# Optimization experiments

Measured on AMD Instinct MI355X. Metric: run time of the kernel, lower is better.

## Reference

```python
import jax, jax.numpy as jnp
import numpy as np

C = 1.0          # Poincare ball curvature
H = 8            # num_heads
EPS = 1e-15
DELTA = 1e-7
SC = np.sqrt(C)  # sqrt curvature


def _norm(x):
    return jnp.sqrt(jnp.clip(jnp.sum(x * x, -1, keepdims=True), 1e-15))


def mobius_add(x, y):
    xy = jnp.sum(x * y, -1, keepdims=True)
    x2 = jnp.sum(x * x, -1, keepdims=True)
    y2 = jnp.sum(y * y, -1, keepdims=True)
    num = (1 + 2 * C * xy + C * y2) * x + (1 - C * x2) * y
    den = 1 + 2 * C * xy + C * C * x2 * y2
    return num / (den + EPS)


def mobius_matvec(W, x):
    xn = _norm(x)
    mx = x @ W.T
    mxn = _norm(mx)
    arg = jnp.clip(SC * xn, None, 1 - 1e-5)
    return jnp.tanh(mxn / xn * jnp.arctanh(arg)) * mx / (mxn * SC)


def logmap0(x):
    xn = _norm(x)
    return jnp.arctanh(jnp.clip(SC * xn, None, 1 - 1e-5)) * x / (SC * xn)


def expmap0(u):
    un = _norm(u)
    return jnp.tanh(SC * un) * u / (SC * un)


def hyp_linear(W, b, x):
    return mobius_add(mobius_matvec(W, x), b)


def setup_inputs() -> dict:
    key = jax.random.key(0)
    ks = jax.random.split(key, 5)
    B, S, E = 2, 512, 256
    x = jax.random.normal(ks[0], (B, S, E), jnp.float32) * 0.02  # inside unit ball
    scale = float(np.sqrt(6.0 / (E + E)))  # xavier uniform bound
    Wq = jax.random.uniform(ks[1], (E, E), jnp.float32, -scale, scale)
    Wk = jax.random.uniform(ks[2], (E, E), jnp.float32, -scale, scale)
    Wv = jax.random.uniform(ks[3], (E, E), jnp.float32, -scale, scale)
    Wo = jax.random.uniform(ks[4], (E, E), jnp.float32, -scale, scale)
    z = jnp.zeros((E,), jnp.float32)
    head_scaling = jnp.ones((H, 1, 1), jnp.float32)
    return {"x": x, "Wq": Wq, "bq": z, "Wk": Wk, "bk": z, "Wv": Wv, "bv": z,
            "Wo": Wo, "bo": z, "head_scaling": head_scaling}


def reference(x, Wq, bq, Wk, bk, Wv, bv, Wo, bo, head_scaling):
    B, S, E = x.shape
    D = E // H
    q = hyp_linear(Wq, bq, x).reshape(B, S, H, D).transpose(0, 2, 1, 3)  # (B,H,S,D)
    k = hyp_linear(Wk, bk, x).reshape(B, S, H, D).transpose(0, 2, 1, 3)
    v = hyp_linear(Wv, bv, x).reshape(B, S, H, D).transpose(0, 2, 1, 3)
    max_norm = (1 - 1e-5) / SC
    q = jnp.minimum(q, max_norm)  # elementwise clamp_max, faithful to source
    k = jnp.minimum(k, max_norm)
    qn = C * jnp.sum(q * q, -1)[..., :, None]   # (B,H,Sq,1)
    kn = C * jnp.sum(k * k, -1)[..., None, :]   # (B,H,1,Sk)
    # pairwise mobius_add(-k, q): (B,H,Sq,Sk,D)
    diff = mobius_add(-k[:, :, None, :, :], q[:, :, :, None, :])
    dn = C * jnp.sum(diff * diff, -1)           # (B,H,Sq,Sk)
    denom = (1 - qn) * (1 - kn) + EPS
    a = jnp.maximum(1 + 2 * dn / denom, 1 + DELTA)
    dist = jnp.log(a + jnp.sqrt(a * a - 1))     # acosh
    scores = -dist / (head_scaling * np.sqrt(D))
    w = jax.nn.softmax(scores, -1)
    out = expmap0(jnp.einsum('bhqk,bhkd->bhqd', w, logmap0(v)))
    out = out.transpose(0, 2, 1, 3).reshape(B, S, E)
    return hyp_linear(Wo, bo, out)
```

## Files before the change

kernel.cpp:

```cpp
#include <hip/hip_runtime.h>
#include <math.h>

#define Ec 256
#define Sc 512
#define Bc 2
#define Hc 8
#define Dc 32
#define MAXNORM (1.0f - 1e-5f)
#define NEc (Bc * Sc * Ec)
#define KSPLIT 2
#define NROWS (Bc * Hc * Sc)

__device__ __forceinline__ float fullWaveSum(float v) {
#pragma unroll
  for (int m = 32; m >= 1; m >>= 1) v += __shfl_xor(v, m, 64);
  return v;
}
__device__ __forceinline__ float halfWaveSum(float v) {
#pragma unroll
  for (int m = 16; m >= 1; m >>= 1) v += __shfl_xor(v, m, 64);
  return v;
}
__device__ __forceinline__ float atanh_fast(float z) {
  return 0.5f * __logf((1.0f + z) / (1.0f - z));
}
__device__ __forceinline__ float tanh_fast(float a) {
  float e = __expf(-2.0f * a);
  return (1.0f - e) / (1.0f + e);
}

__global__ __launch_bounds__(128) void gemm_xwt(
    const float* __restrict__ X,
    const float* __restrict__ W0, const float* __restrict__ W1,
    const float* __restrict__ W2,
    float* __restrict__ O0, float* __restrict__ O1, float* __restrict__ O2) {
  const int tid = threadIdx.x;
  const int bx = blockIdx.x;
  const int by = blockIdx.y;
  const int kz = blockIdx.z;
  const int mat = by >> 2;
  const int cb0 = (by & 3) * 64;
  const int rb0 = bx * 32;
  const float* __restrict__ W = (mat == 0) ? W0 : (mat == 1) ? W1 : W2;
  float* __restrict__ O = ((mat == 0) ? O0 : (mat == 1) ? O1 : O2) + (size_t)kz * NEc;

  __shared__ float Xs[64][36];
  __shared__ float Ws[64][68];

  const int f4 = tid & 15;
  const int sub = tid >> 4;
  const int ty = tid >> 4;
  const int tx = tid & 15;

  float acc[4][4];
#pragma unroll
  for (int i = 0; i < 4; ++i)
#pragma unroll
    for (int j = 0; j < 4; ++j) acc[i][j] = 0.f;

  for (int kk = kz * 128; kk < kz * 128 + 128; kk += 64) {
    __syncthreads();
#pragma unroll
    for (int i = 0; i < 4; ++i) {
      int row = sub + i * 8;
      float4 v = *(const float4*)&X[(size_t)(rb0 + row) * Ec + kk + f4 * 4];
      Xs[f4 * 4 + 0][row] = v.x;
      Xs[f4 * 4 + 1][row] = v.y;
      Xs[f4 * 4 + 2][row] = v.z;
      Xs[f4 * 4 + 3][row] = v.w;
    }
#pragma unroll
    for (int i = 0; i < 8; ++i) {
      int col = sub + i * 8;
      float4 v = *(const float4*)&W[(size_t)(cb0 + col) * Ec + kk + f4 * 4];
      Ws[f4 * 4 + 0][col] = v.x;
      Ws[f4 * 4 + 1][col] = v.y;
      Ws[f4 * 4 + 2][col] = v.z;
      Ws[f4 * 4 + 3][col] = v.w;
    }
    __syncthreads();
#pragma unroll 8
    for (int k = 0; k < 64; ++k) {
      float4 a = *(const float4*)&Xs[k][ty * 4];
      float4 b = *(const float4*)&Ws[k][tx * 4];
      float av[4] = {a.x, a.y, a.z, a.w};
      float bv[4] = {b.x, b.y, b.z, b.w};
#pragma unroll
      for (int i = 0; i < 4; ++i)
#pragma unroll
        for (int j = 0; j < 4; ++j) acc[i][j] = fmaf(av[i], bv[j], acc[i][j]);
    }
  }
#pragma unroll
  for (int i = 0; i < 4; ++i) {
    float4 o = make_float4(acc[i][0], acc[i][1], acc[i][2], acc[i][3]);
    *(float4*)&O[(size_t)(rb0 + ty * 4 + i) * Ec + cb0 + tx * 4] = o;
  }
}

__global__ __launch_bounds__(256) void qkv_stats(
    const float* __restrict__ x,
    const float* __restrict__ mxq, const float* __restrict__ mxk,
    const float* __restrict__ mxv,
    const float* __restrict__ bq, const float* __restrict__ bk,
    const float* __restrict__ bv,
    float* __restrict__ qo, float* __restrict__ ko, float* __restrict__ lvo,
    float* __restrict__ qno, float* __restrict__ kno) {
  const int t = threadIdx.x;
  const int row = blockIdx.x;
  const int b = row >> 9;
  const int s = row & (Sc - 1);
  const size_t idx = (size_t)row * Ec + t;
  const float xv = x[idx];
  float mq = 0.f, mk = 0.f, mv = 0.f;
#pragma unroll
  for (int p = 0; p < KSPLIT; ++p) {
    mq += mxq[idx + (size_t)p * NEc];
    mk += mxk[idx + (size_t)p * NEc];
    mv += mxv[idx + (size_t)p * NEc];
  }
  const float bb[3] = {bq[t], bk[t], bv[t]};
  const float mvals[3] = {mq, mk, mv};

  float vals[10] = {xv * xv,
                    mq * mq, mq * bb[0], bb[0] * bb[0],
                    mk * mk, mk * bb[1], bb[1] * bb[1],
                    mv * mv, mv * bb[2], bb[2] * bb[2]};
  __shared__ float red[10][4];
  __shared__ float fin[10];
#pragma unroll
  for (int i = 0; i < 10; ++i) {
    float v = fullWaveSum(vals[i]);
    if ((t & 63) == 0) red[i][t >> 6] = v;
  }
  __syncthreads();
  if (t < 10) fin[t] = red[t][0] + red[t][1] + red[t][2] + red[t][3];
  __syncthreads();

  const float x2 = fin[0];
  const float xn = sqrtf(fmaxf(x2, 1e-15f));
  const float at = atanh_fast(fminf(xn, MAXNORM));
  const int h = t >> 5;

#pragma unroll
  for (int m = 0; m < 3; ++m) {
    float mx2 = fin[1 + 3 * m];
    float mxb = fin[2 + 3 * m];
    float b2 = fin[3 + 3 * m];
    float mxn = sqrtf(fmaxf(mx2, 1e-15f));
    float scl = tanh_fast((mxn / xn) * at) / mxn;
    float mvv = scl * mvals[m];
    float X2 = scl * scl * mx2;
    float XY = scl * mxb;
    float numc = 1.0f + 2.0f * XY + b2;
    float den = 1.0f + 2.0f * XY + X2 * b2 + 1e-15f;
    float res = (numc * mvv + (1.0f - X2) * bb[m]) / den;
    if (m < 2) {
      res = fminf(res, MAXNORM);
      float s2 = halfWaveSum(res * res);
      if (m == 0) {
        qo[idx] = res;
        if ((t & 31) == 0) qno[(b * Hc + h) * Sc + s] = s2;
      } else {
        ko[idx] = res;
        if ((t & 31) == 0) kno[(b * Hc + h) * Sc + s] = s2;
      }
    } else {
      float vn2 = halfWaveSum(res * res);
      float vn = sqrtf(fmaxf(vn2, 1e-15f));
      float f = atanh_fast(fminf(vn, MAXNORM)) / vn;
      lvo[idx] = f * res;
    }
  }
}

__global__ __launch_bounds__(512) void attn_fused(
    const float* __restrict__ q, const float* __restrict__ k,
    const float* __restrict__ lv, const float* __restrict__ qn,
    const float* __restrict__ kn, const float* __restrict__ hs,
    float* __restrict__ out) {
  const int tid = threadIdx.x;
  const int qt = blockIdx.x;
  const int bh = blockIdx.y;
  const int b = bh >> 3;
  const int h = bh & 7;
  const int sq0 = qt * 32;

  __shared__ float Qs[32][32];
  __shared__ float Ks[256][32];
  __shared__ float lvs[256][36];
  __shared__ float Ps[32][260];
  __shared__ float accm[32][8][32];
  __shared__ float lsb[32][8];

  const int ty = tid >> 6;
  const int tx = tid & 63;
  const int js = tid >> 6;
  const int rg = (tid >> 3) & 7;
  const int dq = tid & 7;

  if (tid < 256) {
    int r = tid >> 3, fd = tid & 7;
    int fsw = fd ^ ((r >> 2) & 7);
    *(float4*)&Qs[r][fsw * 4] =
        *(const float4*)&q[(size_t)(b * Sc + sq0 + r) * Ec + h * Dc + fd * 4];
  }
  const float sinv = -1.0f / (hs[h] * sqrtf((float)Dc));
  float qnv[4];
#pragma unroll
  for (int i = 0; i < 4; ++i) qnv[i] = qn[bh * Sc + sq0 + ty * 4 + i];

  float4 oacc[4];
#pragma unroll
  for (int i = 0; i < 4; ++i) oacc[i] = make_float4(0.f, 0.f, 0.f, 0.f);
  float lsum4[4] = {0.f, 0.f, 0.f, 0.f};

#pragma unroll 1
  for (int kt = 0; kt < 2; ++kt) {
    const int k0 = kt * 256;
    __syncthreads();
#pragma unroll
    for (int i = 0; i < 4; ++i) {
      int qi = tid + i * 512;
      int r = qi >> 3, fd = qi & 7;
      int fsw = fd ^ ((r >> 2) & 7);
      *(float4*)&Ks[r][fsw * 4] =
          *(const float4*)&k[(size_t)(b * Sc + k0 + r) * Ec + h * Dc + fd * 4];
      *(float4*)&lvs[r][fd * 4] =
          *(const float4*)&lv[(size_t)(b * Sc + k0 + r) * Ec + h * Dc + fd * 4];
    }
    float knv[4];
#pragma unroll
    for (int j = 0; j < 4; ++j) knv[j] = kn[bh * Sc + k0 + tx * 4 + j];
    __syncthreads();

    float acc[4][4];
#pragma unroll
    for (int i = 0; i < 4; ++i)
#pragma unroll
      for (int j = 0; j < 4; ++j) acc[i][j] = 0.f;
#pragma unroll
    for (int fd = 0; fd < 8; ++fd) {
      const int qsw = (fd ^ (ty & 7)) * 4;
      const int ksw = (fd ^ (tx & 7)) * 4;
      float4 a[4], bb[4];
#pragma unroll
      for (int i = 0; i < 4; ++i) a[i] = *(const float4*)&Qs[ty * 4 + i][qsw];
#pragma unroll
      for (int j = 0; j < 4; ++j) bb[j] = *(const float4*)&Ks[tx * 4 + j][ksw];
#pragma unroll
      for (int i = 0; i < 4; ++i)
#pragma unroll
        for (int j = 0; j < 4; ++j) {
          acc[i][j] = fmaf(a[i].x, bb[j].x, acc[i][j]);
          acc[i][j] = fmaf(a[i].y, bb[j].y, acc[i][j]);
          acc[i][j] = fmaf(a[i].z, bb[j].z, acc[i][j]);
          acc[i][j] = fmaf(a[i].w, bb[j].w, acc[i][j]);
        }
    }
#pragma unroll
    for (int i = 0; i < 4; ++i) {
      const float q2 = qnv[i];
      const float omq = 1.0f - q2;
      float po[4];
#pragma unroll
      for (int j = 0; j < 4; ++j) {
        const float k2 = knv[j];
        const float kq = acc[i][j];
        const float omk = 1.0f - k2;
        float s2x2 = fmaf(-4.0f, kq, 2.0f * k2 + 2.0f * q2);
        float dden = fmaf(k2, q2, fmaf(-2.0f, kq, 1.0f)) + 1e-15f;
        float Pd = fmaf(dden, omk * omq, 1e-20f);
        float rp = __builtin_amdgcn_rcpf(Pd);
        float tt = fmaxf(s2x2 * rp, 1e-7f);
        float z = (1.0f + tt) + sqrtf(fmaf(tt, tt, tt + tt));
        po[j] = __builtin_amdgcn_exp2f(sinv * __builtin_amdgcn_logf(z));
      }
      float4 o4 = make_float4(po[0], po[1], po[2], po[3]);
      *(float4*)&Ps[ty * 4 + i][tx * 4] = o4;
    }
    __syncthreads();

#pragma unroll
    for (int jq = 0; jq < 8; ++jq) {
      const int j0 = js * 32 + jq * 4;
      float4 p[4], l[4];
#pragma unroll
      for (int i = 0; i < 4; ++i) p[i] = *(const float4*)&Ps[rg * 4 + i][j0];
#pragma unroll
      for (int c = 0; c < 4; ++c) l[c] = *(const float4*)&lvs[j0 + c][dq * 4];
#pragma unroll
      for (int i = 0; i < 4; ++i) {
        lsum4[i] += (p[i].x + p[i].y) + (p[i].z + p[i].w);
        oacc[i].x = fmaf(p[i].x, l[0].x, oacc[i].x);
        oacc[i].y = fmaf(p[i].x, l[0].y, oacc[i].y);
        oacc[i].z = fmaf(p[i].x, l[0].z, oacc[i].z);
        oacc[i].w = fmaf(p[i].x, l[0].w, oacc[i].w);
        oacc[i].x = fmaf(p[i].y, l[1].x, oacc[i].x);
        oacc[i].y = fmaf(p[i].y, l[1].y, oacc[i].y);
        oacc[i].z = fmaf(p[i].y, l[1].z, oacc[i].z);
        oacc[i].w = fmaf(p[i].y, l[1].w, oacc[i].w);
        oacc[i].x = fmaf(p[i].z, l[2].x, oacc[i].x);
        oacc[i].y = fmaf(p[i].z, l[2].y, oacc[i].y);
        oacc[i].z = fmaf(p[i].z, l[2].z, oacc[i].z);
        oacc[i].w = fmaf(p[i].z, l[2].w, oacc[i].w);
        oacc[i].x = fmaf(p[i].w, l[3].x, oacc[i].x);
        oacc[i].y = fmaf(p[i].w, l[3].y, oacc[i].y);
        oacc[i].z = fmaf(p[i].w, l[3].z, oacc[i].z);
        oacc[i].w = fmaf(p[i].w, l[3].w, oacc[i].w);
      }
    }
  }

  __syncthreads();
#pragma unroll
  for (int i = 0; i < 4; ++i)
    *(float4*)&accm[rg * 4 + i][js][dq * 4] = oacc[i];
  if (dq == 0) {
#pragma unroll
    for (int i = 0; i < 4; ++i) lsb[rg * 4 + i][js] = lsum4[i];
  }
  __syncthreads();

  if (tid < 256) {
    const int rw = tid >> 3;
    const int d2 = tid & 7;
    float4 o = make_float4(0.f, 0.f, 0.f, 0.f);
    float ls = 0.f;
#pragma unroll
    for (int g = 0; g < 8; ++g) {
      float4 a4 = *(const float4*)&accm[rw][g][d2 * 4];
      o.x += a4.x; o.y += a4.y; o.z += a4.z; o.w += a4.w;
      ls += lsb[rw][g];
    }
    const float li = 1.0f / ls;
    o.x *= li; o.y *= li; o.z *= li; o.w *= li;
    float un2 = fmaf(o.x, o.x, fmaf(o.y, o.y, fmaf(o.z, o.z, o.w * o.w)));
#pragma unroll
    for (int m = 4; m >= 1; m >>= 1) un2 += __shfl_xor(un2, m, 8);
    float un = sqrtf(fmaxf(un2, 1e-15f));
    float f = tanh_fast(un) / un;
    float4 ov = make_float4(o.x * f, o.y * f, o.z * f, o.w * f);
    *(float4*)&out[(size_t)(b * Sc + sq0 + rw) * Ec + h * Dc + d2 * 4] = ov;
  }
}

__global__ __launch_bounds__(256) void proj_stats(
    const float* __restrict__ xin, const float* __restrict__ mx,
    const float* __restrict__ bo, float* __restrict__ out) {
  const int t = threadIdx.x;
  const int row = blockIdx.x;
  const size_t idx = (size_t)row * Ec + t;
  const float xv = xin[idx];
  float m = 0.f;
#pragma unroll
  for (int p = 0; p < KSPLIT; ++p) m += mx[idx + (size_t)p * NEc];
  const float bb = bo[t];
  float vals[4] = {xv * xv, m * m, m * bb, bb * bb};
  __shared__ float red[4][4];
  __shared__ float fin[4];
#pragma unroll
  for (int i = 0; i < 4; ++i) {
    float v = fullWaveSum(vals[i]);
    if ((t & 63) == 0) red[i][t >> 6] = v;
  }
  __syncthreads();
  if (t < 4) fin[t] = red[t][0] + red[t][1] + red[t][2] + red[t][3];
  __syncthreads();

  float x2 = fin[0], mx2 = fin[1], mxb = fin[2], b2 = fin[3];
  float xn = sqrtf(fmaxf(x2, 1e-15f));
  float mxn = sqrtf(fmaxf(mx2, 1e-15f));
  float scl = tanh_fast((mxn / xn) * atanh_fast(fminf(xn, MAXNORM))) / mxn;
  float mvv = scl * m;
  float X2 = scl * scl * mx2;
  float XY = scl * mxb;
  float numc = 1.0f + 2.0f * XY + b2;
  float den = 1.0f + 2.0f * XY + X2 * b2 + 1e-15f;
  out[idx] = (numc * mvv + (1.0f - X2) * bb) / den;
}

extern "C" void kernel_launch(void* const* d_in, const int* in_sizes, int n_in,
                              void* d_out, int out_size, void* d_ws, size_t ws_size,
                              hipStream_t stream) {
  (void)in_sizes; (void)n_in; (void)out_size; (void)ws_size;
  const float* x  = (const float*)d_in[0];
  const float* Wq = (const float*)d_in[1];
  const float* bq = (const float*)d_in[2];
  const float* Wk = (const float*)d_in[3];
  const float* bk = (const float*)d_in[4];
  const float* Wv = (const float*)d_in[5];
  const float* bv = (const float*)d_in[6];
  const float* Wo = (const float*)d_in[7];
  const float* bo = (const float*)d_in[8];
  const float* hs = (const float*)d_in[9];

  float* ws = (float*)d_ws;
  const int NE = NEc;
  const int NH = NROWS;
  float* mxq = ws;
  float* mxk = mxq + KSPLIT * NE;
  float* mxv = mxk + KSPLIT * NE;
  float* mxo = mxv + KSPLIT * NE;
  float* qb  = mxo + KSPLIT * NE;
  float* kb  = qb + NE;
  float* lvb = kb + NE;
  float* aob = lvb + NE;
  float* qnb = aob + NE;
  float* knb = qnb + NH;

  const int M = Bc * Sc;

  gemm_xwt<<<dim3(M / 32, 12, KSPLIT), 128, 0, stream>>>(x, Wq, Wk, Wv, mxq, mxk, mxv);
  qkv_stats<<<M, 256, 0, stream>>>(x, mxq, mxk, mxv, bq, bk, bv,
                                   qb, kb, lvb, qnb, knb);
  attn_fused<<<dim3(16, 16), 512, 0, stream>>>(qb, kb, lvb, qnb, knb, hs, aob);
  gemm_xwt<<<dim3(M / 32, 4, KSPLIT), 128, 0, stream>>>(aob, Wo, Wo, Wo, mxo, mxo, mxo);
  proj_stats<<<M, 256, 0, stream>>>(aob, mxo, bo, (float*)d_out);
}
```

Before: 125.6 us.

## Fuse all stages into one persistent kernel with software grid barriers

Replaces the five separate kernel launches with a single 256-block persistent kernel that runs the QKV GEMM, QKV stats, attention, output GEMM and output stats as phases separated by atomic-counter grid barriers. The goal is to remove per-launch overhead and the gaps between dependent launches. The split-K layout also changes: the QKV GEMM now does the full K range with no split, the output GEMM uses a 4-way split, and attention works on 128-key tiles so everything fits one shared-memory pool. In exchange, some phases leave threads idle, and correctness depends on all 256 blocks being resident at once, with an extra memset launch to reset the barrier counters.

New measurement: 212.8 us. 69.4% more time.

```diff
diff --git a/kernel.cpp b/kernel.cpp
--- a/kernel.cpp
+++ b/kernel.cpp
@@ -8,8 +8,9 @@
 #define Dc 32
 #define MAXNORM (1.0f - 1e-5f)
 #define NEc (Bc * Sc * Ec)
-#define KSPLIT 2
 #define NROWS (Bc * Hc * Sc)
+#define NBLK 256
+#define KP 4
 
 __device__ __forceinline__ float fullWaveSum(float v) {
 #pragma unroll
@@ -29,96 +30,98 @@
   return (1.0f - e) / (1.0f + e);
 }
 
-__global__ __launch_bounds__(128) void gemm_xwt(
-    const float* __restrict__ X,
-    const float* __restrict__ W0, const float* __restrict__ W1,
-    const float* __restrict__ W2,
-    float* __restrict__ O0, float* __restrict__ O1, float* __restrict__ O2) {
-  const int tid = threadIdx.x;
-  const int bx = blockIdx.x;
-  const int by = blockIdx.y;
-  const int kz = blockIdx.z;
-  const int mat = by >> 2;
-  const int cb0 = (by & 3) * 64;
-  const int rb0 = bx * 32;
-  const float* __restrict__ W = (mat == 0) ? W0 : (mat == 1) ? W1 : W2;
-  float* __restrict__ O = ((mat == 0) ? O0 : (mat == 1) ? O1 : O2) + (size_t)kz * NEc;
-
-  __shared__ float Xs[64][36];
-  __shared__ float Ws[64][68];
-
-  const int f4 = tid & 15;
-  const int sub = tid >> 4;
-  const int ty = tid >> 4;
-  const int tx = tid & 15;
-
+__device__ __forceinline__ void gridBarrier(unsigned* ctr) {
+  __syncthreads();
+  if (threadIdx.x == 0) {
+    __threadfence();
+    __hip_atomic_fetch_add(ctr, 1u, __ATOMIC_RELAXED, __HIP_MEMORY_SCOPE_AGENT);
+    while (__hip_atomic_load(ctr, __ATOMIC_RELAXED, __HIP_MEMORY_SCOPE_AGENT) <
+           (unsigned)NBLK) {
+      __builtin_amdgcn_s_sleep(2);
+    }
+    __threadfence();
+  }
+  __syncthreads();
+}
+
+__device__ __forceinline__ void gemm_tile(
+    const float* __restrict__ X, const float* __restrict__ W,
+    float* __restrict__ O, float* __restrict__ Xs, float* __restrict__ Ws,
+    const int ltid, const int rb0, const int cb0, const int kk0, const int nk,
+    const bool active) {
+  const int f4 = ltid & 15;
+  const int s8 = ltid >> 4;
+  const int ty = ltid >> 4;
+  const int tx = ltid & 15;
   float acc[4][4];
 #pragma unroll
   for (int i = 0; i < 4; ++i)
 #pragma unroll
     for (int j = 0; j < 4; ++j) acc[i][j] = 0.f;
 
-  for (int kk = kz * 128; kk < kz * 128 + 128; kk += 64) {
+  for (int c = 0; c < nk; ++c) {
+    const int kk = kk0 + c * 64;
     __syncthreads();
+    if (active) {
+#pragma unroll
+      for (int i = 0; i < 4; ++i) {
+        int row = s8 + i * 8;
+        float4 v = *(const float4*)&X[(size_t)(rb0 + row) * Ec + kk + f4 * 4];
+        Xs[(f4 * 4 + 0) * 36 + row] = v.x;
+        Xs[(f4 * 4 + 1) * 36 + row] = v.y;
+        Xs[(f4 * 4 + 2) * 36 + row] = v.z;
+        Xs[(f4 * 4 + 3) * 36 + row] = v.w;
+      }
+#pragma unroll
+      for (int i = 0; i < 8; ++i) {
+        int col = s8 + i * 8;
+        float4 v = *(const float4*)&W[(size_t)(cb0 + col) * Ec + kk + f4 * 4];
+        Ws[(f4 * 4 + 0) * 68 + col] = v.x;
+        Ws[(f4 * 4 + 1) * 68 + col] = v.y;
+        Ws[(f4 * 4 + 2) * 68 + col] = v.z;
+        Ws[(f4 * 4 + 3) * 68 + col] = v.w;
+      }
+    }
+    __syncthreads();
+    if (active) {
+#pragma unroll 8
+      for (int k = 0; k < 64; ++k) {
+        float4 a = *(const float4*)&Xs[k * 36 + ty * 4];
+        float4 b = *(const float4*)&Ws[k * 68 + tx * 4];
+        float av[4] = {a.x, a.y, a.z, a.w};
+        float bv[4] = {b.x, b.y, b.z, b.w};
+#pragma unroll
+        for (int i = 0; i < 4; ++i)
+#pragma unroll
+          for (int j = 0; j < 4; ++j) acc[i][j] = fmaf(av[i], bv[j], acc[i][j]);
+      }
+    }
+  }
+  if (active) {
 #pragma unroll
     for (int i = 0; i < 4; ++i) {
-      int row = sub + i * 8;
-      float4 v = *(const float4*)&X[(size_t)(rb0 + row) * Ec + kk + f4 * 4];
-      Xs[f4 * 4 + 0][row] = v.x;
-      Xs[f4 * 4 + 1][row] = v.y;
-      Xs[f4 * 4 + 2][row] = v.z;
-      Xs[f4 * 4 + 3][row] = v.w;
-    }
-#pragma unroll
-    for (int i = 0; i < 8; ++i) {
-      int col = sub + i * 8;
-      float4 v = *(const float4*)&W[(size_t)(cb0 + col) * Ec + kk + f4 * 4];
-      Ws[f4 * 4 + 0][col] = v.x;
-      Ws[f4 * 4 + 1][col] = v.y;
-      Ws[f4 * 4 + 2][col] = v.z;
-      Ws[f4 * 4 + 3][col] = v.w;
-    }
-    __syncthreads();
-#pragma unroll 8
-    for (int k = 0; k < 64; ++k) {
-      float4 a = *(const float4*)&Xs[k][ty * 4];
-      float4 b = *(const float4*)&Ws[k][tx * 4];
-      float av[4] = {a.x, a.y, a.z, a.w};
-      float bv[4] = {b.x, b.y, b.z, b.w};
-#pragma unroll
-      for (int i = 0; i < 4; ++i)
-#pragma unroll
-        for (int j = 0; j < 4; ++j) acc[i][j] = fmaf(av[i], bv[j], acc[i][j]);
-    }
-  }
-#pragma unroll
-  for (int i = 0; i < 4; ++i) {
-    float4 o = make_float4(acc[i][0], acc[i][1], acc[i][2], acc[i][3]);
-    *(float4*)&O[(size_t)(rb0 + ty * 4 + i) * Ec + cb0 + tx * 4] = o;
-  }
-}
-
-__global__ __launch_bounds__(256) void qkv_stats(
+      float4 o = make_float4(acc[i][0], acc[i][1], acc[i][2], acc[i][3]);
+      *(float4*)&O[(size_t)(rb0 + ty * 4 + i) * Ec + cb0 + tx * 4] = o;
+    }
+  }
+}
+
+__device__ __forceinline__ void qkv_stats_row(
     const float* __restrict__ x,
     const float* __restrict__ mxq, const float* __restrict__ mxk,
     const float* __restrict__ mxv,
     const float* __restrict__ bq, const float* __restrict__ bk,
     const float* __restrict__ bv,
     float* __restrict__ qo, float* __restrict__ ko, float* __restrict__ lvo,
-    float* __restrict__ qno, float* __restrict__ kno) {
-  const int t = threadIdx.x;
-  const int row = blockIdx.x;
+    float* __restrict__ qno, float* __restrict__ kno,
+    const int row, const int t, float (*red)[4], float* fin) {
   const int b = row >> 9;
   const int s = row & (Sc - 1);
   const size_t idx = (size_t)row * Ec + t;
   const float xv = x[idx];
-  float mq = 0.f, mk = 0.f, mv = 0.f;
-#pragma unroll
-  for (int p = 0; p < KSPLIT; ++p) {
-    mq += mxq[idx + (size_t)p * NEc];
-    mk += mxk[idx + (size_t)p * NEc];
-    mv += mxv[idx + (size_t)p * NEc];
-  }
+  const float mq = mxq[idx];
+  const float mk = mxk[idx];
+  const float mv = mxv[idx];
   const float bb[3] = {bq[t], bk[t], bv[t]};
   const float mvals[3] = {mq, mk, mv};
 
@@ -126,8 +129,6 @@
                     mq * mq, mq * bb[0], bb[0] * bb[0],
                     mk * mk, mk * bb[1], bb[1] * bb[1],
                     mv * mv, mv * bb[2], bb[2] * bb[2]};
-  __shared__ float red[10][4];
-  __shared__ float fin[10];
 #pragma unroll
   for (int i = 0; i < 10; ++i) {
     float v = fullWaveSum(vals[i]);
@@ -172,193 +173,20 @@
       lvo[idx] = f * res;
     }
   }
-}
-
-__global__ __launch_bounds__(512) void attn_fused(
-    const float* __restrict__ q, const float* __restrict__ k,
-    const float* __restrict__ lv, const float* __restrict__ qn,
-    const float* __restrict__ kn, const float* __restrict__ hs,
-    float* __restrict__ out) {
-  const int tid = threadIdx.x;
-  const int qt = blockIdx.x;
-  const int bh = blockIdx.y;
-  const int b = bh >> 3;
-  const int h = bh & 7;
-  const int sq0 = qt * 32;
-
-  __shared__ float Qs[32][32];
-  __shared__ float Ks[256][32];
-  __shared__ float lvs[256][36];
-  __shared__ float Ps[32][260];
-  __shared__ float accm[32][8][32];
-  __shared__ float lsb[32][8];
-
-  const int ty = tid >> 6;
-  const int tx = tid & 63;
-  const int js = tid >> 6;
-  const int rg = (tid >> 3) & 7;
-  const int dq = tid & 7;
-
-  if (tid < 256) {
-    int r = tid >> 3, fd = tid & 7;
-    int fsw = fd ^ ((r >> 2) & 7);
-    *(float4*)&Qs[r][fsw * 4] =
-        *(const float4*)&q[(size_t)(b * Sc + sq0 + r) * Ec + h * Dc + fd * 4];
-  }
-  const float sinv = -1.0f / (hs[h] * sqrtf((float)Dc));
-  float qnv[4];
-#pragma unroll
-  for (int i = 0; i < 4; ++i) qnv[i] = qn[bh * Sc + sq0 + ty * 4 + i];
-
-  float4 oacc[4];
-#pragma unroll
-  for (int i = 0; i < 4; ++i) oacc[i] = make_float4(0.f, 0.f, 0.f, 0.f);
-  float lsum4[4] = {0.f, 0.f, 0.f, 0.f};
-
-#pragma unroll 1
-  for (int kt = 0; kt < 2; ++kt) {
-    const int k0 = kt * 256;
-    __syncthreads();
-#pragma unroll
-    for (int i = 0; i < 4; ++i) {
-      int qi = tid + i * 512;
-      int r = qi >> 3, fd = qi & 7;
-      int fsw = fd ^ ((r >> 2) & 7);
-      *(float4*)&Ks[r][fsw * 4] =
-          *(const float4*)&k[(size_t)(b * Sc + k0 + r) * Ec + h * Dc + fd * 4];
-      *(float4*)&lvs[r][fd * 4] =
-          *(const float4*)&lv[(size_t)(b * Sc + k0 + r) * Ec + h * Dc + fd * 4];
-    }
-    float knv[4];
-#pragma unroll
-    for (int j = 0; j < 4; ++j) knv[j] = kn[bh * Sc + k0 + tx * 4 + j];
-    __syncthreads();
-
-    float acc[4][4];
-#pragma unroll
-    for (int i = 0; i < 4; ++i)
-#pragma unroll
-      for (int j = 0; j < 4; ++j) acc[i][j] = 0.f;
-#pragma unroll
-    for (int fd = 0; fd < 8; ++fd) {
-      const int qsw = (fd ^ (ty & 7)) * 4;
-      const int ksw = (fd ^ (tx & 7)) * 4;
-      float4 a[4], bb[4];
-#pragma unroll
-      for (int i = 0; i < 4; ++i) a[i] = *(const float4*)&Qs[ty * 4 + i][qsw];
-#pragma unroll
-      for (int j = 0; j < 4; ++j) bb[j] = *(const float4*)&Ks[tx * 4 + j][ksw];
-#pragma unroll
-      for (int i = 0; i < 4; ++i)
-#pragma unroll
-        for (int j = 0; j < 4; ++j) {
-          acc[i][j] = fmaf(a[i].x, bb[j].x, acc[i][j]);
-          acc[i][j] = fmaf(a[i].y, bb[j].y, acc[i][j]);
-          acc[i][j] = fmaf(a[i].z, bb[j].z, acc[i][j]);
-          acc[i][j] = fmaf(a[i].w, bb[j].w, acc[i][j]);
-        }
-    }
-#pragma unroll
-    for (int i = 0; i < 4; ++i) {
-      const float q2 = qnv[i];
-      const float omq = 1.0f - q2;
-      float po[4];
-#pragma unroll
-      for (int j = 0; j < 4; ++j) {
-        const float k2 = knv[j];
-        const float kq = acc[i][j];
-        const float omk = 1.0f - k2;
-        float s2x2 = fmaf(-4.0f, kq, 2.0f * k2 + 2.0f * q2);
-        float dden = fmaf(k2, q2, fmaf(-2.0f, kq, 1.0f)) + 1e-15f;
-        float Pd = fmaf(dden, omk * omq, 1e-20f);
-        float rp = __builtin_amdgcn_rcpf(Pd);
-        float tt = fmaxf(s2x2 * rp, 1e-7f);
-        float z = (1.0f + tt) + sqrtf(fmaf(tt, tt, tt + tt));
-        po[j] = __builtin_amdgcn_exp2f(sinv * __builtin_amdgcn_logf(z));
-      }
-      float4 o4 = make_float4(po[0], po[1], po[2], po[3]);
-      *(float4*)&Ps[ty * 4 + i][tx * 4] = o4;
-    }
-    __syncthreads();
-
-#pragma unroll
-    for (int jq = 0; jq < 8; ++jq) {
-      const int j0 = js * 32 + jq * 4;
-      float4 p[4], l[4];
-#pragma unroll
-      for (int i = 0; i < 4; ++i) p[i] = *(const float4*)&Ps[rg * 4 + i][j0];
-#pragma unroll
-      for (int c = 0; c < 4; ++c) l[c] = *(const float4*)&lvs[j0 + c][dq * 4];
-#pragma unroll
-      for (int i = 0; i < 4; ++i) {
-        lsum4[i] += (p[i].x + p[i].y) + (p[i].z + p[i].w);
-        oacc[i].x = fmaf(p[i].x, l[0].x, oacc[i].x);
-        oacc[i].y = fmaf(p[i].x, l[0].y, oacc[i].y);
-        oacc[i].z = fmaf(p[i].x, l[0].z, oacc[i].z);
-        oacc[i].w = fmaf(p[i].x, l[0].w, oacc[i].w);
-        oacc[i].x = fmaf(p[i].y, l[1].x, oacc[i].x);
-        oacc[i].y = fmaf(p[i].y, l[1].y, oacc[i].y);
-        oacc[i].z = fmaf(p[i].y, l[1].z, oacc[i].z);
-        oacc[i].w = fmaf(p[i].y, l[1].w, oacc[i].w);
-        oacc[i].x = fmaf(p[i].z, l[2].x, oacc[i].x);
-        oacc[i].y = fmaf(p[i].z, l[2].y, oacc[i].y);
-        oacc[i].z = fmaf(p[i].z, l[2].z, oacc[i].z);
-        oacc[i].w = fmaf(p[i].z, l[2].w, oacc[i].w);
-        oacc[i].x = fmaf(p[i].w, l[3].x, oacc[i].x);
-        oacc[i].y = fmaf(p[i].w, l[3].y, oacc[i].y);
-        oacc[i].z = fmaf(p[i].w, l[3].z, oacc[i].z);
-        oacc[i].w = fmaf(p[i].w, l[3].w, oacc[i].w);
-      }
-    }
-  }
-
-  __syncthreads();
-#pragma unroll
-  for (int i = 0; i < 4; ++i)
-    *(float4*)&accm[rg * 4 + i][js][dq * 4] = oacc[i];
-  if (dq == 0) {
-#pragma unroll
-    for (int i = 0; i < 4; ++i) lsb[rg * 4 + i][js] = lsum4[i];
-  }
-  __syncthreads();
-
-  if (tid < 256) {
-    const int rw = tid >> 3;
-    const int d2 = tid & 7;
-    float4 o = make_float4(0.f, 0.f, 0.f, 0.f);
-    float ls = 0.f;
-#pragma unroll
-    for (int g = 0; g < 8; ++g) {
-      float4 a4 = *(const float4*)&accm[rw][g][d2 * 4];
-      o.x += a4.x; o.y += a4.y; o.z += a4.z; o.w += a4.w;
-      ls += lsb[rw][g];
-    }
-    const float li = 1.0f / ls;
-    o.x *= li; o.y *= li; o.z *= li; o.w *= li;
-    float un2 = fmaf(o.x, o.x, fmaf(o.y, o.y, fmaf(o.z, o.z, o.w * o.w)));
-#pragma unroll
-    for (int m = 4; m >= 1; m >>= 1) un2 += __shfl_xor(un2, m, 8);
-    float un = sqrtf(fmaxf(un2, 1e-15f));
-    float f = tanh_fast(un) / un;
-    float4 ov = make_float4(o.x * f, o.y * f, o.z * f, o.w * f);
-    *(float4*)&out[(size_t)(b * Sc + sq0 + rw) * Ec + h * Dc + d2 * 4] = ov;
-  }
-}
-
-__global__ __launch_bounds__(256) void proj_stats(
+  __syncthreads();
+}
+
+__device__ __forceinline__ void proj_stats_row(
     const float* __restrict__ xin, const float* __restrict__ mx,
-    const float* __restrict__ bo, float* __restrict__ out) {
-  const int t = threadIdx.x;
-  const int row = blockIdx.x;
+    const float* __restrict__ bo, float* __restrict__ out,
+    const int row, const int t, float (*red)[4], float* fin) {
   const size_t idx = (size_t)row * Ec + t;
   const float xv = xin[idx];
   float m = 0.f;
 #pragma unroll
-  for (int p = 0; p < KSPLIT; ++p) m += mx[idx + (size_t)p * NEc];
+  for (int p = 0; p < KP; ++p) m += mx[idx + (size_t)p * NEc];
   const float bb = bo[t];
   float vals[4] = {xv * xv, m * m, m * bb, bb * bb};
-  __shared__ float red[4][4];
-  __shared__ float fin[4];
 #pragma unroll
   for (int i = 0; i < 4; ++i) {
     float v = fullWaveSum(vals[i]);
@@ -378,6 +206,253 @@
   float numc = 1.0f + 2.0f * XY + b2;
   float den = 1.0f + 2.0f * XY + X2 * b2 + 1e-15f;
   out[idx] = (numc * mvv + (1.0f - X2) * bb) / den;
+  __syncthreads();
+}
+
+__global__ __launch_bounds__(512) void fused_all(
+    const float* __restrict__ x,
+    const float* __restrict__ Wq, const float* __restrict__ bq,
+    const float* __restrict__ Wk, const float* __restrict__ bk,
+    const float* __restrict__ Wv, const float* __restrict__ bv,
+    const float* __restrict__ Wo, const float* __restrict__ bo,
+    const float* __restrict__ hs,
+    float* __restrict__ mxq, float* __restrict__ mxk, float* __restrict__ mxv,
+    float* __restrict__ mxo, float* __restrict__ qb, float* __restrict__ kb,
+    float* __restrict__ lvb, float* __restrict__ aob, float* __restrict__ qnb,
+    float* __restrict__ knb, float* __restrict__ out, unsigned* bar) {
+  __shared__ float smem[13952];
+  __shared__ float red[2][10][4];
+  __shared__ float fin[2][10];
+  const int tid = threadIdx.x;
+  const int blk = blockIdx.x;
+
+  {
+    const int sub = tid >> 7;
+    const int ltid = tid & 127;
+    const int slot = blk * 2 + (sub & 1);
+    const bool active = (sub < 2) && (slot < 384);
+    const int s = active ? slot : 0;
+    const int mat = s >> 7;
+    const int rem = s & 127;
+    const int cb0 = ((rem >> 5) & 3) * 64;
+    const int rb0 = (rem & 31) * 32;
+    const float* W = (mat == 0) ? Wq : (mat == 1) ? Wk : Wv;
+    float* O = (mat == 0) ? mxq : (mat == 1) ? mxk : mxv;
+    float* Xs = smem + (sub & 1) * 6656;
+    float* Ws = Xs + 2304;
+    gemm_tile(x, W, O, Xs, Ws, ltid, rb0, cb0, 0, 4, active);
+  }
+  gridBarrier(&bar[0]);
+
+  {
+    const int half = tid >> 8;
+    const int t = tid & 255;
+    const int unit = blk * 2 + half;
+#pragma unroll 1
+    for (int iter = 0; iter < 2; ++iter) {
+      qkv_stats_row(x, mxq, mxk, mxv, bq, bk, bv, qb, kb, lvb, qnb, knb,
+                    unit + iter * 512, t, red[half], fin[half]);
+    }
+  }
+  gridBarrier(&bar[1]);
+
+  {
+    const int qt = blk & 15;
+    const int bh = blk >> 4;
+    const int b = bh >> 3;
+    const int h = bh & 7;
+    const int sq0 = qt * 32;
+
+    float* Qs = smem;
+    float* Ks = smem + 1024;
+    float* lvs = smem + 5120;
+    float* Ps = smem + 9728;
+    float* accm = smem + 1024;
+    float* lsb = smem + 9216;
+
+    const int ty = tid >> 6;
+    const int tx = tid & 63;
+    const int js = tid >> 6;
+    const int rg = (tid >> 3) & 7;
+    const int dq = tid & 7;
+
+    if (tid < 256) {
+      int r = tid >> 3, fd = tid & 7;
+      int fsw = fd ^ ((r >> 2) & 7);
+      *(float4*)&Qs[r * 32 + fsw * 4] =
+          *(const float4*)&qb[(size_t)(b * Sc + sq0 + r) * Ec + h * Dc + fd * 4];
+    }
+    const float sinv = -1.0f / (hs[h] * sqrtf((float)Dc));
+    float qnv[4];
+#pragma unroll
+    for (int i = 0; i < 4; ++i) qnv[i] = qnb[bh * Sc + sq0 + ty * 4 + i];
+
+    float4 oacc[4];
+#pragma unroll
+    for (int i = 0; i < 4; ++i) oacc[i] = make_float4(0.f, 0.f, 0.f, 0.f);
+    float lsum4[4] = {0.f, 0.f, 0.f, 0.f};
+
+#pragma unroll 1
+    for (int kt = 0; kt < 4; ++kt) {
+      const int k0 = kt * 128;
+      __syncthreads();
+#pragma unroll
+      for (int i = 0; i < 2; ++i) {
+        int qi = tid + i * 512;
+        int r = qi >> 3, fd = qi & 7;
+        int fsw = fd ^ ((r >> 2) & 7);
+        *(float4*)&Ks[r * 32 + fsw * 4] =
+            *(const float4*)&kb[(size_t)(b * Sc + k0 + r) * Ec + h * Dc + fd * 4];
+        *(float4*)&lvs[r * 36 + fd * 4] =
+            *(const float4*)&lvb[(size_t)(b * Sc + k0 + r) * Ec + h * Dc + fd * 4];
+      }
+      float knv[2];
+#pragma unroll
+      for (int j = 0; j < 2; ++j) knv[j] = knb[bh * Sc + k0 + tx * 2 + j];
+      __syncthreads();
+
+      float acc[4][2];
+#pragma unroll
+      for (int i = 0; i < 4; ++i) {
+        acc[i][0] = 0.f;
+        acc[i][1] = 0.f;
+      }
+#pragma unroll
+      for (int fd = 0; fd < 8; ++fd) {
+        const int qsw = (fd ^ (ty & 7)) * 4;
+        const int ksw = (fd ^ ((tx >> 1) & 7)) * 4;
+        float4 a[4], bb2[2];
+#pragma unroll
+        for (int i = 0; i < 4; ++i)
+          a[i] = *(const float4*)&Qs[(ty * 4 + i) * 32 + qsw];
+#pragma unroll
+        for (int j = 0; j < 2; ++j)
+          bb2[j] = *(const float4*)&Ks[(tx * 2 + j) * 32 + ksw];
+#pragma unroll
+        for (int i = 0; i < 4; ++i)
+#pragma unroll
+          for (int j = 0; j < 2; ++j) {
+            acc[i][j] = fmaf(a[i].x, bb2[j].x, acc[i][j]);
+            acc[i][j] = fmaf(a[i].y, bb2[j].y, acc[i][j]);
+            acc[i][j] = fmaf(a[i].z, bb2[j].z, acc[i][j]);
+            acc[i][j] = fmaf(a[i].w, bb2[j].w, acc[i][j]);
+          }
+      }
+#pragma unroll
+      for (int i = 0; i < 4; ++i) {
+        const float q2 = qnv[i];
+        const float omq = 1.0f - q2;
+        float po[2];
+#pragma unroll
+        for (int j = 0; j < 2; ++j) {
+          const float k2 = knv[j];
+          const float kq = acc[i][j];
+          const float omk = 1.0f - k2;
+          float s2x2 = fmaf(-4.0f, kq, 2.0f * k2 + 2.0f * q2);
+          float dden = fmaf(k2, q2, fmaf(-2.0f, kq, 1.0f)) + 1e-15f;
+          float Pd = fmaf(dden, omk * omq, 1e-20f);
+          float rp = __builtin_amdgcn_rcpf(Pd);
+          float tt = fmaxf(s2x2 * rp, 1e-7f);
+          float z = (1.0f + tt) + sqrtf(fmaf(tt, tt, tt + tt));
+          po[j] = __builtin_amdgcn_exp2f(sinv * __builtin_amdgcn_logf(z));
+        }
+        *(float2*)&Ps[(ty * 4 + i) * 132 + tx * 2] = make_float2(po[0], po[1]);
+      }
+      __syncthreads();
+
+#pragma unroll
+      for (int jq = 0; jq < 4; ++jq) {
+        const int j0 = js * 16 + jq * 4;
+        float4 p[4], l[4];
+#pragma unroll
+        for (int i = 0; i < 4; ++i)
+          p[i] = *(const float4*)&Ps[(rg * 4 + i) * 132 + j0];
+#pragma unroll
+        for (int c = 0; c < 4; ++c)
+          l[c] = *(const float4*)&lvs[(j0 + c) * 36 + dq * 4];
+#pragma unroll
+        for (int i = 0; i < 4; ++i) {
+          lsum4[i] += (p[i].x + p[i].y) + (p[i].z + p[i].w);
+          oacc[i].x = fmaf(p[i].x, l[0].x, oacc[i].x);
+          oacc[i].y = fmaf(p[i].x, l[0].y, oacc[i].y);
+          oacc[i].z = fmaf(p[i].x, l[0].z, oacc[i].z);
+          oacc[i].w = fmaf(p[i].x, l[0].w, oacc[i].w);
+          oacc[i].x = fmaf(p[i].y, l[1].x, oacc[i].x);
+          oacc[i].y = fmaf(p[i].y, l[1].y, oacc[i].y);
+          oacc[i].z = fmaf(p[i].y, l[1].z, oacc[i].z);
+          oacc[i].w = fmaf(p[i].y, l[1].w, oacc[i].w);
+          oacc[i].x = fmaf(p[i].z, l[2].x, oacc[i].x);
+          oacc[i].y = fmaf(p[i].z, l[2].y, oacc[i].y);
+          oacc[i].z = fmaf(p[i].z, l[2].z, oacc[i].z);
+          oacc[i].w = fmaf(p[i].z, l[2].w, oacc[i].w);
+          oacc[i].x = fmaf(p[i].w, l[3].x, oacc[i].x);
+          oacc[i].y = fmaf(p[i].w, l[3].y, oacc[i].y);
+          oacc[i].z = fmaf(p[i].w, l[3].z, oacc[i].z);
+          oacc[i].w = fmaf(p[i].w, l[3].w, oacc[i].w);
+        }
+      }
+    }
+
+    __syncthreads();
+#pragma unroll
+    for (int i = 0; i < 4; ++i)
+      *(float4*)&accm[((rg * 4 + i) * 8 + js) * 32 + dq * 4] = oacc[i];
+    if (dq == 0) {
+#pragma unroll
+      for (int i = 0; i < 4; ++i) lsb[(rg * 4 + i) * 8 + js] = lsum4[i];
+    }
+    __syncthreads();
+
+    if (tid < 256) {
+      const int rw = tid >> 3;
+      const int d2 = tid & 7;
+      float4 o = make_float4(0.f, 0.f, 0.f, 0.f);
+      float ls = 0.f;
+#pragma unroll
+      for (int g = 0; g < 8; ++g) {
+        float4 a4 = *(const float4*)&accm[(rw * 8 + g) * 32 + d2 * 4];
+        o.x += a4.x; o.y += a4.y; o.z += a4.z; o.w += a4.w;
+        ls += lsb[rw * 8 + g];
+      }
+      const float li = 1.0f / ls;
+      o.x *= li; o.y *= li; o.z *= li; o.w *= li;
+      float un2 = fmaf(o.x, o.x, fmaf(o.y, o.y, fmaf(o.z, o.z, o.w * o.w)));
+#pragma unroll
+      for (int m = 4; m >= 1; m >>= 1) un2 += __shfl_xor(un2, m, 8);
+      float un = sqrtf(fmaxf(un2, 1e-15f));
+      float f = tanh_fast(un) / un;
+      float4 ov = make_float4(o.x * f, o.y * f, o.z * f, o.w * f);
+      *(float4*)&aob[(size_t)(b * Sc + sq0 + rw) * Ec + h * Dc + d2 * 4] = ov;
+    }
+  }
+  gridBarrier(&bar[2]);
+
+  {
+    const int sub = tid >> 7;
+    const int ltid = tid & 127;
+    const int slot = blk * 2 + (sub & 1);
+    const bool active = (sub < 2);
+    const int kz = (slot >> 7) & 3;
+    const int rem = slot & 127;
+    const int cb0 = ((rem >> 5) & 3) * 64;
+    const int rb0 = (rem & 31) * 32;
+    float* Xs = smem + (sub & 1) * 6656;
+    float* Ws = Xs + 2304;
+    gemm_tile(aob, Wo, mxo + (size_t)kz * NEc, Xs, Ws, ltid, rb0, cb0,
+              kz * 64, 1, active);
+  }
+  gridBarrier(&bar[3]);
+
+  {
+    const int half = tid >> 8;
+    const int t = tid & 255;
+    const int unit = blk * 2 + half;
+#pragma unroll 1
+    for (int iter = 0; iter < 2; ++iter) {
+      proj_stats_row(aob, mxo, bo, out, unit + iter * 512, t,
+                     red[half], fin[half]);
+    }
+  }
 }
 
 extern "C" void kernel_launch(void* const* d_in, const int* in_sizes, int n_in,
@@ -395,26 +470,22 @@
   const float* bo = (const float*)d_in[8];
   const float* hs = (const float*)d_in[9];
 
-  float* ws = (float*)d_ws;
-  const int NE = NEc;
-  const int NH = NROWS;
+  unsigned* bar = (unsigned*)d_ws;
+  float* ws = (float*)((char*)d_ws + 256);
   float* mxq = ws;
-  float* mxk = mxq + KSPLIT * NE;
-  float* mxv = mxk + KSPLIT * NE;
-  float* mxo = mxv + KSPLIT * NE;
-  float* qb  = mxo + KSPLIT * NE;
-  float* kb  = qb + NE;
-  float* lvb = kb + NE;
-  float* aob = lvb + NE;
-  float* qnb = aob + NE;
-  float* knb = qnb + NH;
-
-  const int M = Bc * Sc;
-
-  gemm_xwt<<<dim3(M / 32, 12, KSPLIT), 128, 0, stream>>>(x, Wq, Wk, Wv, mxq, mxk, mxv);
-  qkv_stats<<<M, 256, 0, stream>>>(x, mxq, mxk, mxv, bq, bk, bv,
-                                   qb, kb, lvb, qnb, knb);
-  attn_fused<<<dim3(16, 16), 512, 0, stream>>>(qb, kb, lvb, qnb, knb, hs, aob);
-  gemm_xwt<<<dim3(M / 32, 4, KSPLIT), 128, 0, stream>>>(aob, Wo, Wo, Wo, mxo, mxo, mxo);
-  proj_stats<<<M, 256, 0, stream>>>(aob, mxo, bo, (float*)d_out);
-}
+  float* mxk = mxq + NEc;
+  float* mxv = mxk + NEc;
+  float* mxo = mxv + NEc;
+  float* qb  = mxo + (size_t)KP * NEc;
+  float* kb  = qb + NEc;
+  float* lvb = kb + NEc;
+  float* aob = lvb + NEc;
+  float* qnb = aob + NEc;
+  float* knb = qnb + NROWS;
+  float* outp = (float*)d_out;
+
+  hipMemsetAsync(bar, 0, 4 * sizeof(unsigned), stream);
+  fused_all<<<NBLK, 512, 0, stream>>>(x, Wq, bq, Wk, bk, Wv, bv, Wo, bo, hs,
+                                      mxq, mxk, mxv, mxo, qb, kb, lvb, aob,
+                                      qnb, knb, outp, bar);
+}
```
